# Kernel optimization log

Measured on AMD Instinct MI355X. Metric: run time of the kernel, lower is better.

## Reference

```python
import jax, jax.numpy as jnp
import numpy as np

B, C, H, W = 4, 128, 64, 64
CQ = C // 8  # query/key channels = 16


def setup_inputs() -> dict:
    key = jax.random.key(0)
    ks = jax.random.split(key, 8)
    s = 0.05
    return {
        "x": jax.random.normal(ks[0], (B, C, H, W), jnp.float32),
        "wq": jax.random.normal(ks[1], (CQ, C), jnp.float32) * s,
        "bq": jax.random.normal(ks[2], (CQ,), jnp.float32) * s,
        "wk": jax.random.normal(ks[3], (CQ, C), jnp.float32) * s,
        "bk": jax.random.normal(ks[4], (CQ,), jnp.float32) * s,
        "wv": jax.random.normal(ks[5], (C, C), jnp.float32) * s,
        "bv": jax.random.normal(ks[6], (C,), jnp.float32) * s,
        # original inits gamma to 0; use small nonzero so attention path is exercised
        "gamma": jax.random.normal(ks[7], (1,), jnp.float32) * 0.1,
    }


def reference(x, wq, bq, wk, bk, wv, bv, gamma):
    b, c, h, w = x.shape
    n = h * w
    xf = x.reshape(b, c, n)  # [B, C, N]
    # 1x1 convs are per-position linear maps over channels
    q = jnp.einsum("qc,bcn->bnq", wq, xf) + bq            # [B, N, Cq]
    k = jnp.einsum("qc,bcn->bqn", wk, xf) + bk[:, None]   # [B, Cq, N]
    v = jnp.einsum("oc,bcn->bon", wv, xf) + bv[:, None]   # [B, C, N]
    # unscaled scores, softmax over keys (last dim), as in the original
    attn = jax.nn.softmax(jnp.einsum("bnq,bqm->bnm", q, k), axis=-1)  # [B, N, N]
    # out = value @ attention^T : out[b,c,n] = sum_m v[b,c,m] * attn[b,n,m]
    out = jnp.einsum("bom,bnm->bon", v, attn)             # [B, C, N]
    return gamma[0] * out.reshape(b, c, h, w) + x
```

## Files before the change

### kernel.cpp

```cpp
#include <hip/hip_runtime.h>
#include <hip/hip_bf16.h>

typedef float f32x4  __attribute__((ext_vector_type(4)));
typedef float f32x16 __attribute__((ext_vector_type(16)));
typedef short s16x8  __attribute__((ext_vector_type(8)));
typedef unsigned int u32;

#define NB 4
#define NC 128
#define NNPOS 4096
#define KSP 8
#define LOG2E 1.44269504088896f

__device__ __forceinline__ short bf16s(float x) {
    __hip_bfloat16 h = __float2bfloat16(x);
    return *reinterpret_cast<short*>(&h);
}
__device__ __forceinline__ int packbf2(float lo, float hi) {
    __hip_bfloat162 t = __float22bfloat162_rn(float2{lo, hi});
    return *reinterpret_cast<int*>(&t);
}
__device__ __forceinline__ float bf2f(unsigned short u) {
    unsigned int v = ((unsigned int)u) << 16;
    return *reinterpret_cast<float*>(&v);
}
__device__ __forceinline__ float exp2fast(float x) {
    return __builtin_amdgcn_exp2f(x);
}
__device__ __forceinline__ void gload_lds16(const short* g, short* l) {
    __builtin_amdgcn_global_load_lds(
        (const __attribute__((address_space(1))) u32*)g,
        (__attribute__((address_space(3))) u32*)l, 16, 0, 0);
}

__global__ __launch_bounds__(256) void qkv_kernel(
    const float* __restrict__ x,
    const float* __restrict__ wq, const float* __restrict__ bq,
    const float* __restrict__ wk, const float* __restrict__ bk,
    const float* __restrict__ wv, const float* __restrict__ bv,
    short* __restrict__ qb, short* __restrict__ kb, short* __restrict__ vt)
{
    const int n0  = blockIdx.x * 32;
    const int b   = blockIdx.y;
    const int tid = threadIdx.x;
    const int w = tid >> 6, lane = tid & 63, quad = lane >> 4, nn = lane & 15;

    __shared__ __align__(16) short xsT[32 * 136];
    __shared__ __align__(16) short vstage[4096];

    #pragma unroll
    for (int p = 0; p < 4; ++p) {
        int idx = tid + p * 256;
        int cc = idx >> 3, n4 = (idx & 7) * 4;
        f32x4 xv = *(const f32x4*)&x[((size_t)(b * NC + cc)) * NNPOS + n0 + n4];
        #pragma unroll
        for (int j = 0; j < 4; ++j)
            xsT[(n4 + j) * 136 + cc] = bf16s(xv[j]);
    }

    s16x8 af[3][4];
    bool  live[3];
    f32x4 biasv[3];
    #pragma unroll
    for (int t = 0; t < 3; ++t) {
        int rid = 3 * w + t;
        int R   = rid * 16;
        const float* wsrc = nullptr; const float* bsrc = nullptr; int row0 = 0;
        float scale = 1.0f;
        if (rid < 8)        { wsrc = wv; bsrc = bv; row0 = R; }
        else if (rid == 8)  { wsrc = wq; bsrc = bq; row0 = 0; scale = LOG2E; }
        else if (rid == 10) { wsrc = wk; bsrc = bk; row0 = 0; }
        live[t] = (wsrc != nullptr);
        #pragma unroll
        for (int r = 0; r < 4; ++r)
            biasv[t][r] = live[t] ? scale * bsrc[row0 + quad * 4 + r] : 0.0f;
        if (live[t]) {
            #pragma unroll
            for (int ks = 0; ks < 4; ++ks) {
                const float* src = wsrc + (size_t)(row0 + nn) * NC + ks * 32 + quad * 8;
                f32x4 wa = *(const f32x4*)src;
                f32x4 wb = *(const f32x4*)(src + 4);
                s16x8 f;
                #pragma unroll
                for (int j = 0; j < 4; ++j) {
                    f[j]     = bf16s(scale * wa[j]);
                    f[j + 4] = bf16s(scale * wb[j]);
                }
                af[t][ks] = f;
            }
        }
    }
    __syncthreads();

    f32x4 acc[3][2];
    #pragma unroll
    for (int t = 0; t < 3; ++t)
        #pragma unroll
        for (int nt = 0; nt < 2; ++nt)
            acc[t][nt] = biasv[t];

    #pragma unroll
    for (int nt = 0; nt < 2; ++nt) {
        s16x8 bf[4];
        #pragma unroll
        for (int ks = 0; ks < 4; ++ks)
            bf[ks] = *(const s16x8*)&xsT[(nt * 16 + nn) * 136 + ks * 32 + quad * 8];
        #pragma unroll
        for (int t = 0; t < 3; ++t)
            if (live[t])
                #pragma unroll
                for (int ks = 0; ks < 4; ++ks)
                    acc[t][nt] = __builtin_amdgcn_mfma_f32_16x16x32_bf16(af[t][ks], bf[ks], acc[t][nt], 0, 0, 0);
    }

    const int slot = (nn & 3) | ((nn & 4) << 1) | ((nn & 8) >> 1);

    #pragma unroll
    for (int t = 0; t < 3; ++t) {
        if (!live[t]) continue;
        const int rid = 3 * w + t;
        #pragma unroll
        for (int nt = 0; nt < 2; ++nt) {
            if (rid < 8) {
                #pragma unroll
                for (int r = 0; r < 4; ++r) {
                    int row = rid * 16 + quad * 4 + r;
                    vstage[(((nt << 2) | (row >> 5)) << 9) +
                           ((slot >> 3) << 8) + ((row & 31) << 3) + (slot & 7)]
                        = bf16s(acc[t][nt][r]);
                }
            } else {
                short4 pk;
                pk.x = bf16s(acc[t][nt][0]);
                pk.y = bf16s(acc[t][nt][1]);
                pk.z = bf16s(acc[t][nt][2]);
                pk.w = bf16s(acc[t][nt][3]);
                int n = n0 + nt * 16 + nn;
                short* dst = (rid == 8 ? qb : kb) +
                             ((size_t)(b * NNPOS) + n) * 16 + quad * 4;
                *reinterpret_cast<short4*>(dst) = pk;
            }
        }
    }
    __syncthreads();

    {
        short* vdst = vt + ((size_t)(b * 256) + (n0 >> 4)) * 2048;
        #pragma unroll
        for (int p = 0; p < 2; ++p) {
            int off = (tid + p * 256) * 8;
            *(s16x8*)&vdst[off] = *(const s16x8*)&vstage[off];
        }
    }
}

__global__ __launch_bounds__(256, 2) void attn_kernel(
    const short* __restrict__ qb, const short* __restrict__ kb,
    const short* __restrict__ vt,
    unsigned short* __restrict__ Ow, float* __restrict__ lw)
{
    const int s   = blockIdx.x;
    const int b   = blockIdx.z;
    const int tid = threadIdx.x;
    const int w = tid >> 6, lane = tid & 63, h = lane >> 5, c31 = lane & 31;

    const int q0 = (blockIdx.y * 4 + w) * 64;

    __shared__ __align__(16) short vlds[2][8192];

    s16x8 bqA = *(const s16x8*)(qb + ((size_t)(b * NNPOS) + q0      + c31) * 16 + h * 8);
    s16x8 bqB = *(const s16x8*)(qb + ((size_t)(b * NNPOS) + q0 + 32 + c31) * 16 + h * 8);

    f32x16 acc[2][4];
    #pragma unroll
    for (int t = 0; t < 2; ++t)
        #pragma unroll
        for (int ct = 0; ct < 4; ++ct)
            #pragma unroll
            for (int r = 0; r < 16; ++r) acc[t][ct][r] = 0.0f;
    float lpA0 = 0.f, lpA1 = 0.f, lpB0 = 0.f, lpB1 = 0.f;

    const short* kbp = kb + (size_t)(b * NNPOS) * 16;
    const int mbase  = s * (NNPOS / KSP);
    const short* vtile = vt + (size_t)b * (NC * NNPOS) + ((size_t)(mbase >> 4) << 11);

    f32x16 z;
    #pragma unroll
    for (int r = 0; r < 16; ++r) z[r] = 0.0f;

    #pragma unroll
    for (int j = 0; j < 4; ++j)
        gload_lds16(vtile + (tid << 3) + (j << 11),
                    &vlds[0][0] + (tid << 3) + (j << 11));
    int m0 = mbase;
    s16x8 ak0 = *(const s16x8*)(kbp + (size_t)(m0      + c31) * 16 + h * 8);
    s16x8 ak1 = *(const s16x8*)(kbp + (size_t)(m0 + 32 + c31) * 16 + h * 8);
    __syncthreads();

    int buf = 0;
    #pragma unroll 1
    for (int it = 0; it < NNPOS / KSP / 64; ++it) {
        if (it + 1 < NNPOS / KSP / 64) {
            const short* src = vtile + (((size_t)(it + 1)) << 13);
            short* dst = &vlds[buf ^ 1][0];
            #pragma unroll
            for (int j = 0; j < 4; ++j)
                gload_lds16(src + (tid << 3) + (j << 11),
                            dst + (tid << 3) + (j << 11));
        }

        s16x8 paA[4], paB[4];
        {
            f32x16 s0 = __builtin_amdgcn_mfma_f32_32x32x16_bf16(ak0, bqA, z, 0, 0, 0);
            f32x16 s1 = __builtin_amdgcn_mfma_f32_32x32x16_bf16(ak1, bqA, z, 0, 0, 0);
            #pragma unroll
            for (int p = 0; p < 4; ++p) {
                const f32x16& sv = (p < 2) ? s0 : s1;
                const int off = (p & 1) * 8;
                union { int i[4]; s16x8 v; } u;
                #pragma unroll
                for (int j = 0; j < 4; ++j) {
                    float p0 = exp2fast(sv[off + 2 * j]);
                    float p1 = exp2fast(sv[off + 2 * j + 1]);
                    if (j & 1) lpA1 += p0 + p1; else lpA0 += p0 + p1;
                    u.i[j] = packbf2(p0, p1);
                }
                paA[p] = u.v;
            }
        }
        {
            f32x16 s0 = __builtin_amdgcn_mfma_f32_32x32x16_bf16(ak0, bqB, z, 0, 0, 0);
            f32x16 s1 = __builtin_amdgcn_mfma_f32_32x32x16_bf16(ak1, bqB, z, 0, 0, 0);
            #pragma unroll
            for (int p = 0; p < 4; ++p) {
                const f32x16& sv = (p < 2) ? s0 : s1;
                const int off = (p & 1) * 8;
                union { int i[4]; s16x8 v; } u;
                #pragma unroll
                for (int j = 0; j < 4; ++j) {
                    float p0 = exp2fast(sv[off + 2 * j]);
                    float p1 = exp2fast(sv[off + 2 * j + 1]);
                    if (j & 1) lpB1 += p0 + p1; else lpB0 += p0 + p1;
                    u.i[j] = packbf2(p0, p1);
                }
                paB[p] = u.v;
            }
        }

        if (it + 1 < NNPOS / KSP / 64) {
            m0 += 64;
            ak0 = *(const s16x8*)(kbp + (size_t)(m0      + c31) * 16 + h * 8);
            ak1 = *(const s16x8*)(kbp + (size_t)(m0 + 32 + c31) * 16 + h * 8);
        }

        const short* vb = &vlds[buf][0];
        #pragma unroll
        for (int p = 0; p < 4; ++p)
            #pragma unroll
            for (int ct = 0; ct < 4; ++ct) {
                s16x8 vf = *(const s16x8*)&vb[((p * 4 + ct) << 9) + (lane << 3)];
                acc[0][ct] = __builtin_amdgcn_mfma_f32_32x32x16_bf16(
                    paA[p], vf, acc[0][ct], 0, 0, 0);
                acc[1][ct] = __builtin_amdgcn_mfma_f32_32x32x16_bf16(
                    paB[p], vf, acc[1][ct], 0, 0, 0);
            }

        __syncthreads();
        buf ^= 1;
    }

    float lpA = lpA0 + lpA1;
    float lpB = lpB0 + lpB1;
    lpA += __shfl_xor(lpA, 32, 64);
    lpB += __shfl_xor(lpB, 32, 64);
    if (lane < 32) {
        lw[((size_t)(b * KSP + s)) * NNPOS + q0      + c31] = lpA;
        lw[((size_t)(b * KSP + s)) * NNPOS + q0 + 32 + c31] = lpB;
    }

    #pragma unroll
    for (int ct = 0; ct < 4; ++ct)
        #pragma unroll
        for (int r = 0; r < 16; ++r) {
            int q = q0 + (r & 3) + 8 * (r >> 2) + 4 * h;
            Ow[(((size_t)(b * KSP + s)) * NNPOS + q) * NC + ct * 32 + c31] =
                (unsigned short)bf16s(acc[0][ct][r]);
            Ow[(((size_t)(b * KSP + s)) * NNPOS + q + 32) * NC + ct * 32 + c31] =
                (unsigned short)bf16s(acc[1][ct][r]);
        }
}

__global__ __launch_bounds__(256) void combine_kernel(
    const unsigned short* __restrict__ Ow, const float* __restrict__ lw,
    const float* __restrict__ x, const float* __restrict__ gamma,
    float* __restrict__ out)
{
    const int n0  = blockIdx.x * 64;
    const int b   = blockIdx.y;
    const int tid = threadIdx.x;

    __shared__ float ot[128 * 65 + 64];
    float* lsum = ot + 128 * 65;

    if (tid < 64) {
        float sl = 0.f;
        #pragma unroll
        for (int sI = 0; sI < KSP; ++sI)
            sl += lw[((size_t)(b * KSP + sI)) * NNPOS + n0 + tid];
        lsum[tid] = 1.0f / sl;
    }
    __syncthreads();

    #pragma unroll
    for (int p = 0; p < 4; ++p) {
        int e = tid + p * 256;
        int co = e & 15, n = e >> 4;
        float a[8] = {0.f, 0.f, 0.f, 0.f, 0.f, 0.f, 0.f, 0.f};
        #pragma unroll
        for (int sI = 0; sI < KSP; ++sI) {
            const unsigned short* src = Ow +
                (((size_t)(b * KSP + sI)) * NNPOS + n0 + n) * NC + co * 8;
            union { s16x8 v; unsigned short us[8]; } u;
            u.v = *(const s16x8*)src;
            #pragma unroll
            for (int j = 0; j < 8; ++j) a[j] += bf2f(u.us[j]);
        }
        float inv = lsum[n];
        #pragma unroll
        for (int j = 0; j < 8; ++j)
            ot[(co * 8 + j) * 65 + n] = a[j] * inv;
    }
    __syncthreads();

    const float g = gamma[0];
    #pragma unroll
    for (int p = 0; p < 8; ++p) {
        int e = tid + p * 256;
        int nq = e & 15, c = e >> 4;
        size_t a = ((size_t)(b * NC + c)) * NNPOS + n0 + nq * 4;
        float4 xv = *(const float4*)&x[a];
        float4 o;
        o.x = g * ot[c * 65 + nq * 4]     + xv.x;
        o.y = g * ot[c * 65 + nq * 4 + 1] + xv.y;
        o.z = g * ot[c * 65 + nq * 4 + 2] + xv.z;
        o.w = g * ot[c * 65 + nq * 4 + 3] + xv.w;
        *(float4*)&out[a] = o;
    }
}

extern "C" void kernel_launch(void* const* d_in, const int* in_sizes, int n_in,
                              void* d_out, int out_size, void* d_ws, size_t ws_size,
                              hipStream_t stream) {
    const float* x     = (const float*)d_in[0];
    const float* wq    = (const float*)d_in[1];
    const float* bq    = (const float*)d_in[2];
    const float* wk    = (const float*)d_in[3];
    const float* bk    = (const float*)d_in[4];
    const float* wv    = (const float*)d_in[5];
    const float* bv    = (const float*)d_in[6];
    const float* gamma = (const float*)d_in[7];
    float* out = (float*)d_out;

    short* qb = (short*)d_ws;
    short* kb = qb + (size_t)NB * NNPOS * 16;
    short* vt = kb + (size_t)NB * NNPOS * 16;
    unsigned short* Ow = (unsigned short*)(vt + (size_t)NB * NC * NNPOS);
    float* lw = (float*)(Ow + (size_t)NB * KSP * NNPOS * NC);

    qkv_kernel<<<dim3(128, NB), 256, 0, stream>>>(x, wq, bq, wk, bk, wv, bv, qb, kb, vt);
    attn_kernel<<<dim3(KSP, 16, NB), 256, 0, stream>>>(qb, kb, vt, Ow, lw);
    combine_kernel<<<dim3(NNPOS / 64, NB), 256, 0, stream>>>(Ow, lw, x, gamma, out);
}
```

Before: 113.1 us.

## Fuse split-K combine into attention kernel via last-block atomic counter

Removes the separate combine kernel launch. Each attention block increments a per-(batch, query-tile) counter after writing its partial output, and the last of the KSP split blocks reduces all partials, normalizes and writes the residual output. The counters are zeroed in the qkv kernel. The score exp/pack code is also refactored into a helper that interleaves each score MFMA with its exponentials, which may cut register pressure. The tail work now runs serially in one of eight blocks per tile, which could lengthen the critical path while saving a launch and some scheduling gap.

```diff
diff --git a/kernel.cpp b/kernel.cpp
--- a/kernel.cpp
+++ b/kernel.cpp
@@ -33,17 +33,41 @@
         (__attribute__((address_space(3))) u32*)l, 16, 0, 0);
 }
 
+__device__ __forceinline__ void exppack(const f32x16& sv, s16x8& plo, s16x8& phi,
+                                        float& l0, float& l1) {
+    union { int i[4]; s16x8 v; } u;
+    #pragma unroll
+    for (int j = 0; j < 4; ++j) {
+        float p0 = exp2fast(sv[2 * j]);
+        float p1 = exp2fast(sv[2 * j + 1]);
+        if (j & 1) l1 += p0 + p1; else l0 += p0 + p1;
+        u.i[j] = packbf2(p0, p1);
+    }
+    plo = u.v;
+    #pragma unroll
+    for (int j = 0; j < 4; ++j) {
+        float p0 = exp2fast(sv[8 + 2 * j]);
+        float p1 = exp2fast(sv[8 + 2 * j + 1]);
+        if (j & 1) l1 += p0 + p1; else l0 += p0 + p1;
+        u.i[j] = packbf2(p0, p1);
+    }
+    phi = u.v;
+}
+
 __global__ __launch_bounds__(256) void qkv_kernel(
     const float* __restrict__ x,
     const float* __restrict__ wq, const float* __restrict__ bq,
     const float* __restrict__ wk, const float* __restrict__ bk,
     const float* __restrict__ wv, const float* __restrict__ bv,
-    short* __restrict__ qb, short* __restrict__ kb, short* __restrict__ vt)
+    short* __restrict__ qb, short* __restrict__ kb, short* __restrict__ vt,
+    int* __restrict__ cnt)
 {
     const int n0  = blockIdx.x * 32;
     const int b   = blockIdx.y;
     const int tid = threadIdx.x;
     const int w = tid >> 6, lane = tid & 63, quad = lane >> 4, nn = lane & 15;
+
+    if (blockIdx.x == 0 && tid < 16) cnt[b * 16 + tid] = 0;
 
     __shared__ __align__(16) short xsT[32 * 136];
     __shared__ __align__(16) short vstage[4096];
@@ -157,16 +181,21 @@
 __global__ __launch_bounds__(256, 2) void attn_kernel(
     const short* __restrict__ qb, const short* __restrict__ kb,
     const short* __restrict__ vt,
-    unsigned short* __restrict__ Ow, float* __restrict__ lw)
+    unsigned short* __restrict__ Ow, float* __restrict__ lw,
+    const float* __restrict__ xg, const float* __restrict__ gamma,
+    float* __restrict__ out, int* __restrict__ cnt)
 {
     const int s   = blockIdx.x;
+    const int qy  = blockIdx.y;
     const int b   = blockIdx.z;
     const int tid = threadIdx.x;
     const int w = tid >> 6, lane = tid & 63, h = lane >> 5, c31 = lane & 31;
 
-    const int q0 = (blockIdx.y * 4 + w) * 64;
-
-    __shared__ __align__(16) short vlds[2][8192];
+    const int q0 = (qy * 4 + w) * 64;
+
+    __shared__ __align__(16) char smem[33536];
+    short (*vlds)[8192] = (short (*)[8192])smem;
+    __shared__ int isLast;
 
     s16x8 bqA = *(const s16x8*)(qb + ((size_t)(b * NNPOS) + q0      + c31) * 16 + h * 8);
     s16x8 bqB = *(const s16x8*)(qb + ((size_t)(b * NNPOS) + q0 + 32 + c31) * 16 + h * 8);
@@ -211,40 +240,14 @@
 
         s16x8 paA[4], paB[4];
         {
-            f32x16 s0 = __builtin_amdgcn_mfma_f32_32x32x16_bf16(ak0, bqA, z, 0, 0, 0);
-            f32x16 s1 = __builtin_amdgcn_mfma_f32_32x32x16_bf16(ak1, bqA, z, 0, 0, 0);
-            #pragma unroll
-            for (int p = 0; p < 4; ++p) {
-                const f32x16& sv = (p < 2) ? s0 : s1;
-                const int off = (p & 1) * 8;
-                union { int i[4]; s16x8 v; } u;
-                #pragma unroll
-                for (int j = 0; j < 4; ++j) {
-                    float p0 = exp2fast(sv[off + 2 * j]);
-                    float p1 = exp2fast(sv[off + 2 * j + 1]);
-                    if (j & 1) lpA1 += p0 + p1; else lpA0 += p0 + p1;
-                    u.i[j] = packbf2(p0, p1);
-                }
-                paA[p] = u.v;
-            }
-        }
-        {
-            f32x16 s0 = __builtin_amdgcn_mfma_f32_32x32x16_bf16(ak0, bqB, z, 0, 0, 0);
-            f32x16 s1 = __builtin_amdgcn_mfma_f32_32x32x16_bf16(ak1, bqB, z, 0, 0, 0);
-            #pragma unroll
-            for (int p = 0; p < 4; ++p) {
-                const f32x16& sv = (p < 2) ? s0 : s1;
-                const int off = (p & 1) * 8;
-                union { int i[4]; s16x8 v; } u;
-                #pragma unroll
-                for (int j = 0; j < 4; ++j) {
-                    float p0 = exp2fast(sv[off + 2 * j]);
-                    float p1 = exp2fast(sv[off + 2 * j + 1]);
-                    if (j & 1) lpB1 += p0 + p1; else lpB0 += p0 + p1;
-                    u.i[j] = packbf2(p0, p1);
-                }
-                paB[p] = u.v;
-            }
+            f32x16 sc = __builtin_amdgcn_mfma_f32_32x32x16_bf16(ak0, bqA, z, 0, 0, 0);
+            exppack(sc, paA[0], paA[1], lpA0, lpA1);
+            sc = __builtin_amdgcn_mfma_f32_32x32x16_bf16(ak1, bqA, z, 0, 0, 0);
+            exppack(sc, paA[2], paA[3], lpA0, lpA1);
+            sc = __builtin_amdgcn_mfma_f32_32x32x16_bf16(ak0, bqB, z, 0, 0, 0);
+            exppack(sc, paB[0], paB[1], lpB0, lpB1);
+            sc = __builtin_amdgcn_mfma_f32_32x32x16_bf16(ak1, bqB, z, 0, 0, 0);
+            exppack(sc, paB[2], paB[3], lpB0, lpB1);
         }
 
         if (it + 1 < NNPOS / KSP / 64) {
@@ -288,63 +291,68 @@
             Ow[(((size_t)(b * KSP + s)) * NNPOS + q + 32) * NC + ct * 32 + c31] =
                 (unsigned short)bf16s(acc[1][ct][r]);
         }
-}
-
-__global__ __launch_bounds__(256) void combine_kernel(
-    const unsigned short* __restrict__ Ow, const float* __restrict__ lw,
-    const float* __restrict__ x, const float* __restrict__ gamma,
-    float* __restrict__ out)
-{
-    const int n0  = blockIdx.x * 64;
-    const int b   = blockIdx.y;
-    const int tid = threadIdx.x;
-
-    __shared__ float ot[128 * 65 + 64];
+
+    __threadfence();
+    if (tid == 0) {
+        int old = atomicAdd(&cnt[b * 16 + qy], 1);
+        isLast = (old == KSP - 1);
+    }
+    __syncthreads();
+    if (!isLast) return;
+    __threadfence();
+
+    float* ot   = (float*)smem;
     float* lsum = ot + 128 * 65;
-
-    if (tid < 64) {
-        float sl = 0.f;
-        #pragma unroll
-        for (int sI = 0; sI < KSP; ++sI)
-            sl += lw[((size_t)(b * KSP + sI)) * NNPOS + n0 + tid];
-        lsum[tid] = 1.0f / sl;
-    }
-    __syncthreads();
-
-    #pragma unroll
-    for (int p = 0; p < 4; ++p) {
-        int e = tid + p * 256;
-        int co = e & 15, n = e >> 4;
-        float a[8] = {0.f, 0.f, 0.f, 0.f, 0.f, 0.f, 0.f, 0.f};
-        #pragma unroll
-        for (int sI = 0; sI < KSP; ++sI) {
-            const unsigned short* src = Ow +
-                (((size_t)(b * KSP + sI)) * NNPOS + n0 + n) * NC + co * 8;
-            union { s16x8 v; unsigned short us[8]; } u;
-            u.v = *(const s16x8*)src;
-            #pragma unroll
-            for (int j = 0; j < 8; ++j) a[j] += bf2f(u.us[j]);
-        }
-        float inv = lsum[n];
-        #pragma unroll
-        for (int j = 0; j < 8; ++j)
-            ot[(co * 8 + j) * 65 + n] = a[j] * inv;
-    }
-    __syncthreads();
-
     const float g = gamma[0];
-    #pragma unroll
-    for (int p = 0; p < 8; ++p) {
-        int e = tid + p * 256;
-        int nq = e & 15, c = e >> 4;
-        size_t a = ((size_t)(b * NC + c)) * NNPOS + n0 + nq * 4;
-        float4 xv = *(const float4*)&x[a];
-        float4 o;
-        o.x = g * ot[c * 65 + nq * 4]     + xv.x;
-        o.y = g * ot[c * 65 + nq * 4 + 1] + xv.y;
-        o.z = g * ot[c * 65 + nq * 4 + 2] + xv.z;
-        o.w = g * ot[c * 65 + nq * 4 + 3] + xv.w;
-        *(float4*)&out[a] = o;
+
+    #pragma unroll 1
+    for (int tI = 0; tI < 4; ++tI) {
+        const int n0c = qy * 256 + tI * 64;
+
+        if (tid < 64) {
+            float sl = 0.f;
+            #pragma unroll
+            for (int sI = 0; sI < KSP; ++sI)
+                sl += lw[((size_t)(b * KSP + sI)) * NNPOS + n0c + tid];
+            lsum[tid] = 1.0f / sl;
+        }
+        __syncthreads();
+
+        #pragma unroll
+        for (int p = 0; p < 4; ++p) {
+            int e = tid + p * 256;
+            int co = e & 15, n = e >> 4;
+            float a[8] = {0.f, 0.f, 0.f, 0.f, 0.f, 0.f, 0.f, 0.f};
+            #pragma unroll
+            for (int sI = 0; sI < KSP; ++sI) {
+                const unsigned short* src = Ow +
+                    (((size_t)(b * KSP + sI)) * NNPOS + n0c + n) * NC + co * 8;
+                union { s16x8 v; unsigned short us[8]; } u;
+                u.v = *(const s16x8*)src;
+                #pragma unroll
+                for (int j = 0; j < 8; ++j) a[j] += bf2f(u.us[j]);
+            }
+            float inv = lsum[n];
+            #pragma unroll
+            for (int j = 0; j < 8; ++j)
+                ot[(co * 8 + j) * 65 + n] = a[j] * inv;
+        }
+        __syncthreads();
+
+        #pragma unroll
+        for (int p = 0; p < 8; ++p) {
+            int e = tid + p * 256;
+            int nq = e & 15, c = e >> 4;
+            size_t a = ((size_t)(b * NC + c)) * NNPOS + n0c + nq * 4;
+            float4 xv = *(const float4*)&xg[a];
+            float4 o;
+            o.x = g * ot[c * 65 + nq * 4]     + xv.x;
+            o.y = g * ot[c * 65 + nq * 4 + 1] + xv.y;
+            o.z = g * ot[c * 65 + nq * 4 + 2] + xv.z;
+            o.w = g * ot[c * 65 + nq * 4 + 3] + xv.w;
+            *(float4*)&out[a] = o;
+        }
+        __syncthreads();
     }
 }
 
@@ -366,8 +374,8 @@
     short* vt = kb + (size_t)NB * NNPOS * 16;
     unsigned short* Ow = (unsigned short*)(vt + (size_t)NB * NC * NNPOS);
     float* lw = (float*)(Ow + (size_t)NB * KSP * NNPOS * NC);
-
-    qkv_kernel<<<dim3(128, NB), 256, 0, stream>>>(x, wq, bq, wk, bk, wv, bv, qb, kb, vt);
-    attn_kernel<<<dim3(KSP, 16, NB), 256, 0, stream>>>(qb, kb, vt, Ow, lw);
-    combine_kernel<<<dim3(NNPOS / 64, NB), 256, 0, stream>>>(Ow, lw, x, gamma, out);
-}
+    int* cnt = (int*)(lw + (size_t)NB * KSP * NNPOS);
+
+    qkv_kernel<<<dim3(128, NB), 256, 0, stream>>>(x, wq, bq, wk, bk, wv, bv, qb, kb, vt, cnt);
+    attn_kernel<<<dim3(KSP, 16, NB), 256, 0, stream>>>(qb, kb, vt, Ow, lw, x, gamma, out, cnt);
+}
```

New measurement: 213.4 us. 88.7% more time.
